# Kernel optimization log

Hardware: AMD Instinct MI355X
Metric: run time of the kernel (lower is better)

The kernel has to match this reference:

```python
import jax, jax.numpy as jnp
import numpy as np

HID, HEADS, NL, WIN = 512, 4, 2, 5
DH = HID // HEADS
SLOPE = 0.2
EPS = 1e-5
B, L = 16, 1024
NEG_INF = -1e30


def _layer_norm(x, g, b):
    m = jnp.mean(x, axis=-1, keepdims=True)
    v = jnp.mean(jnp.square(x - m), axis=-1, keepdims=True)
    return (x - m) * jax.lax.rsqrt(v + EPS) * g + b


def _build_masks(attention_mask, last_starts, seq_len):
    # node layout: [g, h_1..h_T, l], total N = seq_len + 2
    bsz = attention_mask.shape[0]
    N = seq_len + 2
    pos = jnp.arange(N)
    last = last_starts[:, None, None]  # (B,1,1)
    global_mask = jnp.ones((bsz, 1, N), jnp.float32)
    # local node: g, itself, and tokens of the last utterance (node idx last+1 .. seq_len)
    local_mask = ((pos == 0) | (pos == N - 1) | ((pos >= last + 1) & (pos <= seq_len))).astype(jnp.float32)  # (B,1,N)
    # token nodes: global node + window of neighboring tokens
    ii = jnp.arange(seq_len)[:, None]          # query token index
    jj = jnp.arange(N)[None, :]                # key node index
    t = jj - 1                                 # token index of key node (valid in [0, seq_len))
    win = (t >= 0) & (t < seq_len) & (jnp.abs(ii - t) <= WIN)
    base = (jj == 0) | win                     # (L,N)
    # tokens at/after last utterance start also attend to the local node
    to_local = (jnp.arange(seq_len)[None, :, None] >= last_starts[:, None, None]) & (jj[None] == N - 1)  # (B,L,N)
    token_mask = (base[None] | to_local).astype(jnp.float32)
    # padding: key tokens masked by attention_mask; g and l always visible; padded queries fully masked
    ones_col = jnp.ones((bsz, seq_len, 1), jnp.float32)
    pad = jnp.concatenate([ones_col, jnp.broadcast_to(attention_mask[:, None, :], (bsz, seq_len, seq_len)), ones_col], axis=-1)
    token_mask = token_mask * pad * attention_mask[:, :, None]
    return global_mask, local_mask, token_mask


def _gat(q, kv, W, a, mask):
    # W: (hid, hid) as torch Linear weight (out,in); a: (H, 2*DH)
    bsz, Lq, _ = q.shape
    N = kv.shape[1]
    Q = (q @ W.T).reshape(bsz, Lq, HEADS, DH)
    K = (kv @ W.T).reshape(bsz, N, HEADS, DH)
    V = K  # key==value tensor in this module, same projection
    # additive score decomposes: (a . [Q||K]) = Q.a_q + K.a_k
    sq = jnp.einsum('bqhd,hd->bhq', Q, a[:, :DH])
    sk = jnp.einsum('bkhd,hd->bhk', K, a[:, DH:])
    s = sq[:, :, :, None] + sk[:, :, None, :]           # (B,H,Lq,N)
    s = jnp.where(s >= 0, s, SLOPE * s)                 # LeakyReLU
    s = jnp.where(mask[:, None, :, :] > 0, s, NEG_INF)
    w = jax.nn.softmax(s, axis=-1)
    w = jnp.where(jnp.isnan(w), 0.0, w)
    out = jnp.einsum('bhqk,bkhd->bqhd', w, V)
    return out.reshape(bsz, Lq, HID)


def setup_inputs() -> dict:
    key = jax.random.key(0)
    ks = jax.random.split(key, 10)
    scale = 1.0 / np.sqrt(HID)
    return {
        'global_embedding': jax.random.normal(ks[0], (B, HID), jnp.float32),
        'token_embeddings': jax.random.normal(ks[1], (B, L, HID), jnp.float32),
        'local_embedding': jax.random.normal(ks[2], (B, HID), jnp.float32),
        'attention_mask': jnp.ones((B, L), jnp.float32),
        'last_utterance_starts': jax.random.randint(ks[3], (B,), 0, 512, jnp.int32),
        'gat_W': jax.random.normal(ks[4], (NL, HID, HID), jnp.float32) * scale,
        'gat_a': jax.random.normal(ks[5], (NL, HEADS, 2 * DH), jnp.float32) * scale,
        'ln_gamma': jnp.ones((NL, HID), jnp.float32),
        'ln_beta': jnp.zeros((NL, HID), jnp.float32),
        'ffn_w1': jax.random.normal(ks[6], (3, HID, 4 * HID), jnp.float32) * scale,
        'ffn_b1': jnp.zeros((3, 4 * HID), jnp.float32),
        'ffn_w2': jax.random.normal(ks[7], (3, 4 * HID, HID), jnp.float32) * (1.0 / np.sqrt(4 * HID)),
        'ffn_b2': jnp.zeros((3, HID), jnp.float32),
        'out_ln_gamma': jnp.ones((3, HID), jnp.float32),
        'out_ln_beta': jnp.zeros((3, HID), jnp.float32),
    }


def reference(global_embedding, token_embeddings, local_embedding, attention_mask,
              last_utterance_starts, gat_W, gat_a, ln_gamma, ln_beta,
              ffn_w1, ffn_b1, ffn_w2, ffn_b2, out_ln_gamma, out_ln_beta):
    bsz, seq_len, _ = token_embeddings.shape
    gm, lm, tm = _build_masks(attention_mask, last_utterance_starts, seq_len)
    g = global_embedding[:, None, :]
    h = token_embeddings
    l = local_embedding[:, None, :]
    nodes = jnp.concatenate([g, h, l], axis=1)
    for k in range(NL):
        g_new = jax.nn.elu(_gat(g, nodes, gat_W[k], gat_a[k], gm))
        h_new = jax.nn.elu(_gat(h, nodes, gat_W[k], gat_a[k], tm))
        l_new = jax.nn.elu(_gat(l, nodes, gat_W[k], gat_a[k], lm))
        g = _layer_norm(g + g_new, ln_gamma[k], ln_beta[k])
        h = _layer_norm(h + h_new, ln_gamma[k], ln_beta[k])
        l = _layer_norm(l + l_new, ln_gamma[k], ln_beta[k])
        nodes = jnp.concatenate([g, h, l], axis=1)
    def ffn(x, i):
        hmid = jax.nn.gelu(x @ ffn_w1[i] + ffn_b1[i], approximate=False)
        return hmid @ ffn_w2[i] + ffn_b2[i]
    g = g + ffn(g, 0)
    h = h + ffn(h, 1)
    l = l + ffn(l, 2)
    updated_global = _layer_norm(g[:, 0], out_ln_gamma[0], out_ln_beta[0])
    updated_tokens = _layer_norm(h, out_ln_gamma[1], out_ln_beta[1])
    updated_local = _layer_norm(l[:, 0], out_ln_gamma[2], out_ln_beta[2])
    return updated_global, updated_tokens, updated_local
```

## Files before the change

### kernel.cpp

```cpp
#include <hip/hip_runtime.h>
#include <stdint.h>
#include <math.h>

#define HIDN 512
#define NHEAD 4
#define DHEAD 128
#define BATCH 16
#define SEQ 1024
#define NNODE 1026
#define MROWS (BATCH * NNODE)
#define MPAD 16512
#define MTOK (BATCH * SEQ)
#define FFD 2048
#define JCH 114

typedef short bf16x8 __attribute__((ext_vector_type(8)));
typedef float f32x4 __attribute__((ext_vector_type(4)));

__device__ __forceinline__ float bf2f(ushort u) {
    union { uint32_t i; float f; } v; v.i = ((uint32_t)u) << 16; return v.f;
}
__device__ __forceinline__ ushort f2bf(float f) {
    uint32_t x = __float_as_uint(f);
    return (ushort)((x + 0x7fffu + ((x >> 16) & 1u)) >> 16);
}
__device__ __forceinline__ float gelu(float v) {
    float z = v * 0.70710678118654752f;
    float az = fabsf(z);
    float t = __builtin_amdgcn_rcpf(1.f + 0.3275911f * az);
    float y = ((((1.061405429f * t - 1.453152027f) * t + 1.421413741f) * t
                - 0.284496736f) * t + 0.254829592f) * t;
    float e = __expf(-az * az);
    float erfv = 1.f - y * e;
    erfv = (z >= 0.f) ? erfv : -erfv;
    return 0.5f * v * (1.f + erfv);
}
__device__ __forceinline__ int cswz(int row, int col) {
    return row * 128 + ((((col >> 2) ^ (row & 7)) & 31) << 2) + (col & 3);
}

__global__ __launch_bounds__(256) void k_build_nodes(
    const float* __restrict__ g, const float* __restrict__ tok,
    const float* __restrict__ l, ushort* __restrict__ nb)
{
    int idx = blockIdx.x * 256 + threadIdx.x;
    int r = idx >> 9, c = idx & 511;
    float u = 0.f;
    if (r < MROWS) {
        int b = r / NNODE;
        int n = r - b * NNODE;
        if (n == 0)            u = g[b * HIDN + c];
        else if (n <= SEQ)     u = tok[((size_t)b * SEQ + (n - 1)) * HIDN + c];
        else                   u = l[b * HIDN + c];
    }
    nb[idx] = f2bf(u);
}

__global__ __launch_bounds__(256) void k_cvt(
    const float* __restrict__ in, ushort* __restrict__ out, int n)
{
    int idx = blockIdx.x * 256 + threadIdx.x;
    if (idx < n) out[idx] = f2bf(in[idx]);
}

__global__ __launch_bounds__(256) void k_transpose(
    const float* __restrict__ in, ushort* __restrict__ out, int R, int C)
{
    __shared__ float t[32][33];
    int x = blockIdx.x * 32 + threadIdx.x;
    int y0 = blockIdx.y * 32;
    for (int dy = threadIdx.y; dy < 32; dy += 8)
        t[dy][threadIdx.x] = in[(size_t)(y0 + dy) * C + x];
    __syncthreads();
    int ox = y0 + threadIdx.x;
    int oy0 = blockIdx.x * 32;
    for (int dy = threadIdx.y; dy < 32; dy += 8)
        out[(size_t)(oy0 + dy) * R + ox] = f2bf(t[threadIdx.x][dy]);
}

#define BM 128
#define BN 128
#define BK 64

__global__ __launch_bounds__(256) void k_gemm_bt(
    const ushort* __restrict__ A, const ushort* __restrict__ Bt,
    float* __restrict__ Cf, ushort* __restrict__ Cb,
    const float* __restrict__ bias,
    int N, int K, int ldb, int mode, int amap, int mguard, int first)
{
    __shared__ ushort smem[2 * (BM * BK + BN * BK)];
    int tid = threadIdx.x;
    int lane = tid & 63;
    int wave = tid >> 6;
    int wm = wave >> 1, wn = wave & 1;

    int GX = gridDim.x;
    int nwg = GX * gridDim.y;
    int bid = blockIdx.y * GX + blockIdx.x;
    int q = nwg >> 3, r = nwg & 7;
    int xcd = bid & 7, pos = bid >> 3;
    int cbase = (xcd < r) ? xcd * (q + 1) : r * (q + 1) + (xcd - r) * q;
    int wk = cbase + pos;
    int m0 = (wk / GX) * BM;
    int n0 = (wk % GX) * BN;

    f32x4 acc[4][4];
#pragma unroll
    for (int i = 0; i < 4; ++i)
#pragma unroll
        for (int j = 0; j < 4; ++j) acc[i][j] = (f32x4){0.f, 0.f, 0.f, 0.f};

    int lr = lane >> 3;
    int gco = ((lane & 7) ^ lr) * 8;

    const ushort* pA[4];
    const ushort* pB[4];
#pragma unroll
    for (int u = 0; u < 4; ++u) {
        int qq = wave * 4 + u;
        int rr8 = qq * 8 + lr;
        int grA = m0 + rr8;
        if (amap) grA = grA + 2 * (grA >> 10) + 1;
        pA[u] = A + (size_t)grA * K + gco;
        int grB = n0 + rr8;
        pB[u] = Bt + (size_t)grB * ldb + gco;
    }

    auto stage = [&](int buf) {
        ushort* sA = smem + buf * (BM * BK + BN * BK);
        ushort* sB = sA + BM * BK;
#pragma unroll
        for (int u = 0; u < 4; ++u) {
            int qq = wave * 4 + u;
            __builtin_amdgcn_global_load_lds(
                (const __attribute__((address_space(1))) void*)pA[u],
                (__attribute__((address_space(3))) void*)&sA[qq * 512], 16, 0, 0);
            __builtin_amdgcn_global_load_lds(
                (const __attribute__((address_space(1))) void*)pB[u],
                (__attribute__((address_space(3))) void*)&sB[qq * 512], 16, 0, 0);
            pA[u] += BK;
            pB[u] += BK;
        }
    };

    const int nk = K / BK;
    stage(0);
    __syncthreads();

    int rr = lane & 7;
    int rhi = (lane & 15) >> 3;
    for (int t = 0; t < nk; ++t) {
        if (t + 1 < nk) stage((t + 1) & 1);

        const ushort* sAr = smem + (t & 1) * (BM * BK + BN * BK);
        const ushort* sBr = sAr + BM * BK;
#pragma unroll
        for (int kk = 0; kk < BK; kk += 32) {
            int c4 = (kk >> 3) + (lane >> 4);
            int swz = rr * 64 + ((c4 ^ rr) << 3);
            bf16x8 af[4], bfr[4];
#pragma unroll
            for (int i = 0; i < 4; ++i)
                af[i] = *reinterpret_cast<const bf16x8*>(&sAr[(wm * 8 + i * 2 + rhi) * 512 + swz]);
#pragma unroll
            for (int j = 0; j < 4; ++j)
                bfr[j] = *reinterpret_cast<const bf16x8*>(&sBr[(wn * 8 + j * 2 + rhi) * 512 + swz]);
#pragma unroll
            for (int i = 0; i < 4; ++i)
#pragma unroll
                for (int j = 0; j < 4; ++j)
                    acc[i][j] = __builtin_amdgcn_mfma_f32_16x16x32_bf16(af[i], bfr[j], acc[i][j], 0, 0, 0);
        }
        asm volatile("s_waitcnt vmcnt(0)" ::: "memory");
        __builtin_amdgcn_s_barrier();
    }
    __syncthreads();

    float* sC = (float*)smem;
    int rb = (lane >> 4) * 4;
    int cb = lane & 15;
    int lrow = tid >> 2;
    int lcol = (tid & 3) << 5;
#pragma unroll
    for (int pass = 0; pass < 2; ++pass) {
        if (wm == pass) {
#pragma unroll
            for (int i = 0; i < 4; ++i)
#pragma unroll
                for (int j = 0; j < 4; ++j)
#pragma unroll
                    for (int rg = 0; rg < 4; ++rg)
                        sC[cswz(i * 16 + rb + rg, wn * 64 + j * 16 + cb)] = acc[i][j][rg];
        }
        __syncthreads();
        int gm = m0 + pass * 64 + lrow;
        if (gm < mguard) {
            int gn0 = n0 + lcol;
            float v[32];
#pragma unroll
            for (int e4 = 0; e4 < 8; ++e4) {
                float4 t = *(const float4*)&sC[cswz(lrow, lcol + e4 * 4)];
                v[e4 * 4 + 0] = t.x; v[e4 * 4 + 1] = t.y;
                v[e4 * 4 + 2] = t.z; v[e4 * 4 + 3] = t.w;
            }
            if (mode == 1 || mode == 3) {
                if (mode == 3) {
                    const float* a1 = bias + (gn0 >> 7) * 256 + (gn0 & 127);
                    const float* a2 = a1 + 128;
                    float s1 = 0.f, s2 = 0.f;
#pragma unroll
                    for (int j = 0; j < 32; ++j) {
                        s1 += v[j] * a1[j];
                        s2 += v[j] * a2[j];
                    }
                    s1 += __shfl_xor(s1, 1); s1 += __shfl_xor(s1, 2);
                    s2 += __shfl_xor(s2, 1); s2 += __shfl_xor(s2, 2);
                    if ((tid & 3) == 0) {
                        Cf[gm * 4 + (gn0 >> 7)] = s1;
                        Cf[(size_t)MPAD * 4 + gm * 4 + (gn0 >> 7)] = s2;
                    }
                }
                uint4* dst = (uint4*)(Cb + (size_t)gm * N + gn0);
#pragma unroll
                for (int q2 = 0; q2 < 4; ++q2) {
                    float s[8];
#pragma unroll
                    for (int t = 0; t < 8; ++t) {
                        float x = v[q2 * 8 + t];
                        s[t] = (mode == 1) ? gelu(x + bias[gn0 + q2 * 8 + t]) : x;
                    }
                    uint4 w;
                    w.x = (uint32_t)f2bf(s[0]) | ((uint32_t)f2bf(s[1]) << 16);
                    w.y = (uint32_t)f2bf(s[2]) | ((uint32_t)f2bf(s[3]) << 16);
                    w.z = (uint32_t)f2bf(s[4]) | ((uint32_t)f2bf(s[5]) << 16);
                    w.w = (uint32_t)f2bf(s[6]) | ((uint32_t)f2bf(s[7]) << 16);
                    dst[q2] = w;
                }
            } else {
                float4* dst = (float4*)(Cf + (size_t)gm * N + gn0);
#pragma unroll
                for (int e4 = 0; e4 < 8; ++e4) {
                    float4 t;
                    t.x = v[e4 * 4 + 0]; t.y = v[e4 * 4 + 1];
                    t.z = v[e4 * 4 + 2]; t.w = v[e4 * 4 + 3];
                    if (!first) {
                        float4 o = dst[e4];
                        t.x += o.x; t.y += o.y; t.z += o.z; t.w += o.w;
                    }
                    dst[e4] = t;
                }
            }
        }
        __syncthreads();
    }
}

__global__ __launch_bounds__(256) void k_attn_token(
    const ushort* __restrict__ P, const float* __restrict__ sq, const float* __restrict__ sk,
    const float* __restrict__ am, const int* __restrict__ last,
    const float* __restrict__ gam, const float* __restrict__ bet,
    ushort* __restrict__ nb)
{
    int wid = blockIdx.x * 4 + (threadIdx.x >> 6);
    int tokid = ((wid & 7) << 11) | (wid >> 3);
    int b = tokid >> 10, i = tokid & 1023;
    int lane = threadIdx.x & 63;
    int hh = lane >> 4;
    int base = b * NNODE;
    int qrow = base + 1 + i;

    int kr[13];
    int val[13];
    int rowok = am[b * SEQ + i] > 0.f ? 1 : 0;
    kr[0] = base; val[0] = rowok;
#pragma unroll
    for (int s = 0; s < 11; ++s) {
        int t = i - 5 + s;
        int inb = (t >= 0) && (t <= SEQ - 1);
        int tt = inb ? t : 0;
        int v = inb && rowok && (am[b * SEQ + tt] > 0.f);
        kr[1 + s] = base + 1 + tt;
        val[1 + s] = v;
    }
    kr[12] = base + SEQ + 1;
    val[12] = (rowok && (i >= last[b])) ? 1 : 0;

    float sqv = sq[qrow * 4 + hh];
    float sc[13];
    float mx = -1e30f;
#pragma unroll
    for (int t = 0; t < 13; ++t) {
        float s = 0.f;
        if (val[t]) {
            s = sqv + sk[kr[t] * 4 + hh];
            s = s >= 0.f ? s : 0.2f * s;
            mx = fmaxf(mx, s);
        }
        sc[t] = s;
    }
    float den = 0.f;
#pragma unroll
    for (int t = 0; t < 13; ++t) {
        float ev = 0.f;
        if (val[t]) ev = expf(sc[t] - mx);
        sc[t] = ev; den += ev;
    }
    float inv = (den > 1e-30f && den < 1e30f) ? 1.f / den : 0.f;

    int o0 = lane * 8;
    float accv[8] = {0.f, 0.f, 0.f, 0.f, 0.f, 0.f, 0.f, 0.f};
#pragma unroll
    for (int t = 0; t < 13; ++t) {
        if (val[t]) {
            float wgt = sc[t] * inv;
            const ushort* pv = P + (size_t)kr[t] * HIDN + o0;
#pragma unroll
            for (int d = 0; d < 8; ++d) accv[d] += wgt * bf2f(pv[d]);
        }
    }

    ushort* nrow = nb + (size_t)qrow * HIDN + o0;
    float x[8], s1 = 0.f, s2 = 0.f;
#pragma unroll
    for (int d = 0; d < 8; ++d) {
        float v = accv[d];
        v = v > 0.f ? v : expf(v) - 1.f;
        v += bf2f(nrow[d]);
        x[d] = v; s1 += v; s2 += v * v;
    }
#pragma unroll
    for (int off = 32; off; off >>= 1) { s1 += __shfl_xor(s1, off); s2 += __shfl_xor(s2, off); }
    float mean = s1 * (1.f / 512.f);
    float var = s2 * (1.f / 512.f) - mean * mean; var = fmaxf(var, 0.f);
    float rn = rsqrtf(var + 1e-5f);
#pragma unroll
    for (int d = 0; d < 8; ++d) {
        float y = (x[d] - mean) * rn * gam[o0 + d] + bet[o0 + d];
        nrow[d] = f2bf(y);
    }
}

__global__ __launch_bounds__(256) void k_glsm(
    const float* __restrict__ sq, const float* __restrict__ sk,
    const int* __restrict__ last,
    float* __restrict__ ebuf, float* __restrict__ einv)
{
    __shared__ float red[1024];
    int rw = blockIdx.x, b = rw >> 1, isl = rw & 1;
    int base = b * NNODE;
    int qrow = base + (isl ? (SEQ + 1) : 0);
    int lastb = last[b];
    int tid = threadIdx.x;

    float sqh[4];
#pragma unroll
    for (int h = 0; h < 4; ++h) sqh[h] = sq[qrow * 4 + h];

    float mx[4] = {-1e30f, -1e30f, -1e30f, -1e30f};
    for (int j = tid; j < NNODE; j += 256) {
        bool ok = !isl || (j == 0 || j == SEQ + 1 || (j >= lastb + 1 && j <= SEQ));
        if (ok) {
#pragma unroll
            for (int h = 0; h < 4; ++h) {
                float s = sqh[h] + sk[(base + j) * 4 + h];
                s = s >= 0.f ? s : 0.2f * s;
                mx[h] = fmaxf(mx[h], s);
            }
        }
    }
#pragma unroll
    for (int h = 0; h < 4; ++h) red[tid * 4 + h] = mx[h];
    __syncthreads();
    for (int s = 128; s; s >>= 1) {
        if (tid < s) {
#pragma unroll
            for (int h = 0; h < 4; ++h)
                red[tid * 4 + h] = fmaxf(red[tid * 4 + h], red[(tid + s) * 4 + h]);
        }
        __syncthreads();
    }
#pragma unroll
    for (int h = 0; h < 4; ++h) mx[h] = red[h];
    __syncthreads();

    float sm[4] = {0.f, 0.f, 0.f, 0.f};
    for (int j = tid; j < NNODE; j += 256) {
        bool ok = !isl || (j == 0 || j == SEQ + 1 || (j >= lastb + 1 && j <= SEQ));
#pragma unroll
        for (int h = 0; h < 4; ++h) {
            float v = 0.f;
            if (ok) {
                float s = sqh[h] + sk[(base + j) * 4 + h];
                s = s >= 0.f ? s : 0.2f * s;
                v = expf(s - mx[h]);
            }
            ebuf[((size_t)rw * NNODE + j) * 4 + h] = v;
            sm[h] += v;
        }
    }
#pragma unroll
    for (int h = 0; h < 4; ++h) red[tid * 4 + h] = sm[h];
    __syncthreads();
    for (int s = 128; s; s >>= 1) {
        if (tid < s) {
#pragma unroll
            for (int h = 0; h < 4; ++h) red[tid * 4 + h] += red[(tid + s) * 4 + h];
        }
        __syncthreads();
    }
    if (tid < 4) {
        float den = red[tid];
        einv[rw * 4 + tid] = (den > 1e-30f && den < 1e30f) ? 1.f / den : 0.f;
    }
}

__global__ __launch_bounds__(256) void k_glpv(
    const ushort* __restrict__ P, const float* __restrict__ ebuf,
    float* __restrict__ pout2)
{
    __shared__ float es[JCH * 4];
    int p = blockIdx.x, rw = blockIdx.y;
    int b = rw >> 1;
    int base = b * NNODE;
    int tid = threadIdx.x;
    for (int t = tid; t < JCH * 4; t += 256)
        es[t] = ebuf[((size_t)rw * NNODE + p * JCH) * 4 + t];
    __syncthreads();
    int o0 = tid, o1 = tid + 256;
    int h0 = o0 >> 7, h1 = o1 >> 7;
    const ushort* Pb = P + (size_t)(base + p * JCH) * HIDN;
    float a0 = 0.f, a1 = 0.f;
    for (int j = 0; j < JCH; ++j) {
        const ushort* pr = Pb + (size_t)j * HIDN;
        a0 += es[j * 4 + h0] * bf2f(pr[o0]);
        a1 += es[j * 4 + h1] * bf2f(pr[o1]);
    }
    float* o = pout2 + ((size_t)rw * 9 + p) * HIDN;
    o[o0] = a0;
    o[o1] = a1;
}

__global__ __launch_bounds__(256) void k_glred(
    const float* __restrict__ pout2, const float* __restrict__ einv,
    const float* __restrict__ gam, const float* __restrict__ bet,
    ushort* __restrict__ nb)
{
    __shared__ float red[512];
    int rw = blockIdx.x, b = rw >> 1, isl = rw & 1;
    size_t qrow = (size_t)b * NNODE + (isl ? SEQ + 1 : 0);
    int tid = threadIdx.x;
    float xv[2], s1 = 0.f, s2 = 0.f;
#pragma unroll
    for (int u = 0; u < 2; ++u) {
        int o = tid + u * 256;
        int h = o >> 7;
        float acc = 0.f;
#pragma unroll
        for (int p = 0; p < 9; ++p)
            acc += pout2[((size_t)rw * 9 + p) * HIDN + o];
        acc *= einv[rw * 4 + h];
        float v = acc > 0.f ? acc : expf(acc) - 1.f;
        v += bf2f(nb[qrow * HIDN + o]);
        xv[u] = v; s1 += v; s2 += v * v;
    }
    red[tid] = s1;
    __syncthreads();
    for (int s = 128; s; s >>= 1) { if (tid < s) red[tid] += red[tid + s]; __syncthreads(); }
    float mean = red[0] * (1.f / 512.f);
    __syncthreads();
    red[tid] = s2;
    __syncthreads();
    for (int s = 128; s; s >>= 1) { if (tid < s) red[tid] += red[tid + s]; __syncthreads(); }
    float var = red[0] * (1.f / 512.f) - mean * mean; var = fmaxf(var, 0.f);
    float rn = rsqrtf(var + 1e-5f);
#pragma unroll
    for (int u = 0; u < 2; ++u) {
        int o = tid + u * 256;
        float y = (xv[u] - mean) * rn * gam[o] + bet[o];
        nb[qrow * HIDN + o] = f2bf(y);
    }
}

__global__ __launch_bounds__(256) void k_fgl1(
    const ushort* __restrict__ nb, const float* __restrict__ w1,
    float* __restrict__ pmid)
{
    __shared__ float xs[64];
    int p = blockIdx.x, rw = blockIdx.y;
    int b = rw >> 1, isl = rw & 1;
    int idx = isl ? 2 : 0;
    size_t nrow = (size_t)b * NNODE + (isl ? SEQ + 1 : 0);
    int tid = threadIdx.x;
    if (tid < 64) xs[tid] = bf2f(nb[nrow * HIDN + p * 64 + tid]);
    __syncthreads();
    const float* W1 = w1 + (size_t)idx * HIDN * FFD + (size_t)p * 64 * FFD;
    float acc[8] = {0.f, 0.f, 0.f, 0.f, 0.f, 0.f, 0.f, 0.f};
    for (int ii = 0; ii < 64; ++ii) {
        float xv = xs[ii];
        const float* wrow = W1 + (size_t)ii * FFD + tid;
#pragma unroll
        for (int u = 0; u < 8; ++u) acc[u] += xv * wrow[u * 256];
    }
    float* o = pmid + ((size_t)rw * 8 + p) * FFD + tid;
#pragma unroll
    for (int u = 0; u < 8; ++u) o[u * 256] = acc[u];
}

__global__ __launch_bounds__(256) void k_fgl2(
    const float* __restrict__ pmid, const float* __restrict__ b1,
    float* __restrict__ mid)
{
    int g = blockIdx.x * 256 + threadIdx.x;
    int e4 = g * 4;
    int rw = e4 >> 11;
    int m = e4 & 2047;
    int isl = rw & 1;
    int idx = isl ? 2 : 0;
#pragma unroll
    for (int d = 0; d < 4; ++d) {
        float s = 0.f;
#pragma unroll
        for (int p = 0; p < 8; ++p)
            s += pmid[((size_t)rw * 8 + p) * FFD + m + d];
        s += b1[idx * FFD + m + d];
        mid[(size_t)rw * FFD + m + d] = gelu(s);
    }
}

__global__ __launch_bounds__(256) void k_fgl3(
    const float* __restrict__ mid, const float* __restrict__ w2,
    float* __restrict__ pout)
{
    __shared__ float ms[256];
    int p = blockIdx.x, rw = blockIdx.y;
    int isl = rw & 1;
    int idx = isl ? 2 : 0;
    int tid = threadIdx.x;
    ms[tid] = mid[(size_t)rw * FFD + p * 256 + tid];
    __syncthreads();
    const float* W2 = w2 + (size_t)idx * FFD * HIDN + (size_t)p * 256 * HIDN;
    float a0 = 0.f, a1 = 0.f;
    for (int mm = 0; mm < 256; ++mm) {
        float mv = ms[mm];
        const float* wrow = W2 + (size_t)mm * HIDN + tid;
        a0 += mv * wrow[0];
        a1 += mv * wrow[256];
    }
    float* o = pout + ((size_t)rw * 8 + p) * HIDN + tid;
    o[0] = a0;
    o[256] = a1;
}

__global__ __launch_bounds__(256) void k_fgl4(
    const float* __restrict__ pout, const float* __restrict__ b2,
    const ushort* __restrict__ nb,
    const float* __restrict__ og, const float* __restrict__ obt,
    float* __restrict__ out)
{
    __shared__ float red[512];
    int rw = blockIdx.x;
    int b = rw >> 1, isl = rw & 1;
    int idx = isl ? 2 : 0;
    size_t nrow = (size_t)b * NNODE + (isl ? SEQ + 1 : 0);
    int tid = threadIdx.x;
    float xv[2], s1 = 0.f, s2 = 0.f;
#pragma unroll
    for (int u = 0; u < 2; ++u) {
        int o = tid + u * 256;
        float s = 0.f;
#pragma unroll
        for (int p = 0; p < 8; ++p)
            s += pout[((size_t)rw * 8 + p) * HIDN + o];
        s += b2[idx * HIDN + o] + bf2f(nb[nrow * HIDN + o]);
        xv[u] = s; s1 += s; s2 += s * s;
    }
    red[tid] = s1;
    __syncthreads();
    for (int s = 128; s; s >>= 1) { if (tid < s) red[tid] += red[tid + s]; __syncthreads(); }
    float mean = red[0] * (1.f / 512.f);
    __syncthreads();
    red[tid] = s2;
    __syncthreads();
    for (int s = 128; s; s >>= 1) { if (tid < s) red[tid] += red[tid + s]; __syncthreads(); }
    float var = red[0] * (1.f / 512.f) - mean * mean; var = fmaxf(var, 0.f);
    float rn = rsqrtf(var + 1e-5f);
    size_t obase = isl ? ((size_t)8192 + (size_t)MTOK * HIDN + (size_t)b * HIDN)
                       : ((size_t)b * HIDN);
#pragma unroll
    for (int u = 0; u < 2; ++u) {
        int o = tid + u * 256;
        out[obase + o] = (xv[u] - mean) * rn * og[idx * HIDN + o] + obt[idx * HIDN + o];
    }
}

__global__ __launch_bounds__(64) void k_ln_final(
    float* __restrict__ Pt, const ushort* __restrict__ nb,
    const float* __restrict__ b2,
    const float* __restrict__ gam, const float* __restrict__ bet)
{
    int r = blockIdx.x, lane = threadIdx.x;
    int nrow = r + 2 * (r >> 10) + 1;
    int o0 = lane * 8;
    float* x = Pt + (size_t)r * HIDN + o0;
    const ushort* res = nb + (size_t)nrow * HIDN + o0;
    float v[8], s1 = 0.f, s2 = 0.f;
#pragma unroll
    for (int d = 0; d < 8; ++d) {
        float t = x[d] + b2[o0 + d] + bf2f(res[d]);
        v[d] = t; s1 += t; s2 += t * t;
    }
#pragma unroll
    for (int off = 32; off; off >>= 1) { s1 += __shfl_xor(s1, off); s2 += __shfl_xor(s2, off); }
    float mean = s1 * (1.f / 512.f);
    float var = s2 * (1.f / 512.f) - mean * mean; var = fmaxf(var, 0.f);
    float rn = rsqrtf(var + 1e-5f);
#pragma unroll
    for (int d = 0; d < 8; ++d)
        x[d] = (v[d] - mean) * rn * gam[o0 + d] + bet[o0 + d];
}

extern "C" void kernel_launch(void* const* d_in, const int* in_sizes, int n_in,
                              void* d_out, int out_size, void* d_ws, size_t ws_size,
                              hipStream_t stream)
{
    (void)in_sizes; (void)n_in; (void)out_size; (void)ws_size;
    const float* g_emb   = (const float*)d_in[0];
    const float* tok_emb = (const float*)d_in[1];
    const float* l_emb   = (const float*)d_in[2];
    const float* am      = (const float*)d_in[3];
    const int*   last    = (const int*)d_in[4];
    const float* gat_W   = (const float*)d_in[5];
    const float* gat_a   = (const float*)d_in[6];
    const float* ln_g    = (const float*)d_in[7];
    const float* ln_b    = (const float*)d_in[8];
    const float* ffn_w1  = (const float*)d_in[9];
    const float* ffn_b1  = (const float*)d_in[10];
    const float* ffn_w2  = (const float*)d_in[11];
    const float* ffn_b2  = (const float*)d_in[12];
    const float* oln_g   = (const float*)d_in[13];
    const float* oln_b   = (const float*)d_in[14];
    float* out = (float*)d_out;

    char* w = (char*)d_ws;
    ushort* nodes_b = (ushort*)w; w += (size_t)MPAD * HIDN * 2;
    char*   scratch = w;          w += (size_t)8 * 1024 * 1024;
    ushort* w1t     = (ushort*)w; w += (size_t)FFD * HIDN * 2;
    ushort* w2t     = (ushort*)w; w += (size_t)FFD * HIDN * 2;
    ushort* gatWb   = (ushort*)w; w += (size_t)2 * HIDN * HIDN * 2;
    float*  sqb     = (float*)w;  w += (size_t)MPAD * 4 * 4;
    float*  skb     = (float*)w;  w += (size_t)MPAD * 4 * 4;
    ushort* Hmid    = (ushort*)w; w += (size_t)MTOK * FFD * 2;

    float* pmid = (float*)scratch;
    float* mid  = pmid + (size_t)32 * 8 * FFD;
    float* pout = mid + (size_t)32 * FFD;
    float* ebuf  = (float*)(scratch + (size_t)3 * 1024 * 1024);
    float* einv  = ebuf + (size_t)32 * NNODE * 4;
    float* pout2 = einv + 128;

    ushort* P = (ushort*)out;
    float* Pt = out + 8192;

    k_build_nodes<<<MPAD * HIDN / 256, 256, 0, stream>>>(g_emb, tok_emb, l_emb, nodes_b);
    k_cvt<<<(2 * HIDN * HIDN) / 256, 256, 0, stream>>>(gat_W, gatWb, 2 * HIDN * HIDN);
    k_transpose<<<dim3(FFD / 32, HIDN / 32), dim3(32, 8), 0, stream>>>(ffn_w1 + (size_t)HIDN * FFD, w1t, HIDN, FFD);
    k_transpose<<<dim3(HIDN / 32, FFD / 32), dim3(32, 8), 0, stream>>>(ffn_w2 + (size_t)FFD * HIDN, w2t, FFD, HIDN);

    for (int k = 0; k < 2; ++k) {
        k_gemm_bt<<<dim3(HIDN / BN, MPAD / BM), 256, 0, stream>>>(
            nodes_b, gatWb + (size_t)k * HIDN * HIDN, sqb, P,
            gat_a + k * NHEAD * 2 * DHEAD,
            HIDN, HIDN, HIDN, 3, 0, MROWS, 1);
        k_attn_token<<<MTOK / 4, 256, 0, stream>>>(P, sqb, skb, am, last,
                                                   ln_g + k * HIDN, ln_b + k * HIDN, nodes_b);
        k_glsm<<<32, 256, 0, stream>>>(sqb, skb, last, ebuf, einv);
        k_glpv<<<dim3(9, 32), 256, 0, stream>>>(P, ebuf, pout2);
        k_glred<<<32, 256, 0, stream>>>(pout2, einv, ln_g + k * HIDN, ln_b + k * HIDN, nodes_b);
    }

    k_fgl1<<<dim3(8, 32), 256, 0, stream>>>(nodes_b, ffn_w1, pmid);
    k_fgl2<<<64, 256, 0, stream>>>(pmid, ffn_b1, mid);
    k_fgl3<<<dim3(8, 32), 256, 0, stream>>>(mid, ffn_w2, pout);
    k_fgl4<<<32, 256, 0, stream>>>(pout, ffn_b2, nodes_b, oln_g, oln_b, out);

    k_gemm_bt<<<dim3(FFD / BN, MTOK / BM), 256, 0, stream>>>(
        nodes_b, w1t, nullptr, Hmid,
        ffn_b1 + FFD, FFD, HIDN, HIDN, 1, 1, MTOK, 1);
    k_gemm_bt<<<dim3(HIDN / BN, MTOK / BM), 256, 0, stream>>>(
        Hmid, w2t, Pt, nullptr, nullptr,
        HIDN, FFD, FFD, 0, 0, MTOK, 1);
    k_ln_final<<<MTOK, 64, 0, stream>>>(Pt, nodes_b, ffn_b2 + HIDN, oln_g + HIDN, oln_b + HIDN);
}
```

Before: 496.1 us.

## Add 256x256-tile GEMM with direct global-to-LDS loads for token FFN

Introduces a new 512-thread GEMM kernel with 256x256 output tiles, double-buffered LDS staging via global_load_lds, XOR-swizzled shared layout, and a block-index remap for L2 locality. The two token-FFN GEMMs switch to it, fusing bias+GELU in the first. Larger tiles raise arithmetic intensity and cut global traffic, at the cost of 128 KB LDS per block and fewer blocks (the second GEMM launches only 128), which limits occupancy.

```diff
diff --git a/kernel.cpp b/kernel.cpp
--- a/kernel.cpp
+++ b/kernel.cpp
@@ -249,6 +249,162 @@
                     }
                     dst[e4] = t;
                 }
+            }
+        }
+        __syncthreads();
+    }
+}
+
+#define QK 64
+
+__global__ __launch_bounds__(512) void k_gemm256(
+    const ushort* __restrict__ A, const ushort* __restrict__ Bt,
+    float* __restrict__ Cf, ushort* __restrict__ Cb,
+    const float* __restrict__ bias,
+    int N, int K, int mode, int amap)
+{
+    extern __shared__ ushort smem[];
+    int tid = threadIdx.x;
+    int lane = tid & 63;
+    int wave = tid >> 6;
+    int wr = wave >> 2;
+    int wc = wave & 3;
+
+    int GX = gridDim.x;
+    int nwg = GX * gridDim.y;
+    int bid = blockIdx.y * GX + blockIdx.x;
+    int cpx = nwg >> 3;
+    int wk = (bid & 7) * cpx + (bid >> 3);
+    int m0 = (wk / GX) * 256;
+    int n0 = (wk % GX) * 256;
+
+    f32x4 acc[8][4];
+#pragma unroll
+    for (int i = 0; i < 8; ++i)
+#pragma unroll
+        for (int j = 0; j < 4; ++j) acc[i][j] = (f32x4){0.f, 0.f, 0.f, 0.f};
+
+    int lr = lane >> 3;
+    int gco = ((lane & 7) ^ lr) * 8;
+
+    const ushort* pA[4];
+    const ushort* pB[4];
+#pragma unroll
+    for (int u = 0; u < 4; ++u) {
+        int q = wave * 4 + u;
+        int grA = m0 + q * 8 + lr;
+        if (amap) grA = grA + 2 * (grA >> 10) + 1;
+        pA[u] = A + (size_t)grA * K + gco;
+        int grB = n0 + q * 8 + lr;
+        pB[u] = Bt + (size_t)grB * K + gco;
+    }
+
+    auto stage = [&](int buf) {
+        ushort* sA = smem + buf * 32768;
+        ushort* sB = sA + 16384;
+#pragma unroll
+        for (int u = 0; u < 4; ++u) {
+            int q = wave * 4 + u;
+            __builtin_amdgcn_global_load_lds(
+                (const __attribute__((address_space(1))) void*)pA[u],
+                (__attribute__((address_space(3))) void*)&sA[q * 512], 16, 0, 0);
+            __builtin_amdgcn_global_load_lds(
+                (const __attribute__((address_space(1))) void*)pB[u],
+                (__attribute__((address_space(3))) void*)&sB[q * 512], 16, 0, 0);
+            pA[u] += QK;
+            pB[u] += QK;
+        }
+    };
+
+    const int nk = K / QK;
+    stage(0);
+    __syncthreads();
+
+    int rr = lane & 7;
+    int rhi = (lane & 15) >> 3;
+    for (int t = 0; t < nk; ++t) {
+        if (t + 1 < nk) stage((t + 1) & 1);
+
+        const ushort* sAr = smem + (t & 1) * 32768;
+        const ushort* sBr = sAr + 16384;
+#pragma unroll
+        for (int qd = 0; qd < 4; ++qd) {
+            int fi0 = (qd & 1) * 4;
+            int fj0 = (qd >> 1) * 2;
+#pragma unroll
+            for (int kk = 0; kk < 2; ++kk) {
+                int c4 = kk * 4 + (lane >> 4);
+                int swz = rr * 64 + ((c4 ^ rr) << 3);
+                bf16x8 af[4], bfr[2];
+#pragma unroll
+                for (int i = 0; i < 4; ++i) {
+                    int qA = wr * 16 + (fi0 + i) * 2 + rhi;
+                    af[i] = *reinterpret_cast<const bf16x8*>(&sAr[qA * 512 + swz]);
+                }
+#pragma unroll
+                for (int j = 0; j < 2; ++j) {
+                    int qB = wc * 8 + (fj0 + j) * 2 + rhi;
+                    bfr[j] = *reinterpret_cast<const bf16x8*>(&sBr[qB * 512 + swz]);
+                }
+#pragma unroll
+                for (int i = 0; i < 4; ++i)
+#pragma unroll
+                    for (int j = 0; j < 2; ++j)
+                        acc[fi0 + i][fj0 + j] = __builtin_amdgcn_mfma_f32_16x16x32_bf16(
+                            af[i], bfr[j], acc[fi0 + i][fj0 + j], 0, 0, 0);
+            }
+        }
+        __syncthreads();
+    }
+
+    float* sC = (float*)smem;
+    int rb = (lane >> 4) * 4;
+    int cb = lane & 15;
+    int lrow = tid >> 2;
+    int lcol = (tid & 3) << 6;
+#pragma unroll
+    for (int pass = 0; pass < 2; ++pass) {
+        if (wr == pass) {
+#pragma unroll
+            for (int fi = 0; fi < 8; ++fi)
+#pragma unroll
+                for (int fj = 0; fj < 4; ++fj)
+#pragma unroll
+                    for (int rg = 0; rg < 4; ++rg) {
+                        int row = fi * 16 + rb + rg;
+                        int col = wc * 64 + fj * 16 + cb;
+                        sC[row * 256 + ((((col >> 2) ^ (row & 7)) & 63) << 2) + (col & 3)] =
+                            acc[fi][fj][rg];
+                    }
+        }
+        __syncthreads();
+        int gm = m0 + pass * 128 + lrow;
+        if (mode == 1) {
+            uint4* dst = (uint4*)(Cb + (size_t)gm * N + n0 + lcol);
+#pragma unroll
+            for (int g = 0; g < 8; ++g) {
+                int col = lcol + g * 8;
+                float4 a = *(const float4*)&sC[lrow * 256 + ((((col >> 2) ^ (lrow & 7)) & 63) << 2)];
+                float4 b = *(const float4*)&sC[lrow * 256 + (((((col + 4) >> 2) ^ (lrow & 7)) & 63) << 2)];
+                const float* bp = bias + n0 + col;
+                float s0 = gelu(a.x + bp[0]), s1 = gelu(a.y + bp[1]);
+                float s2 = gelu(a.z + bp[2]), s3 = gelu(a.w + bp[3]);
+                float s4 = gelu(b.x + bp[4]), s5 = gelu(b.y + bp[5]);
+                float s6 = gelu(b.z + bp[6]), s7 = gelu(b.w + bp[7]);
+                uint4 w;
+                w.x = (uint32_t)f2bf(s0) | ((uint32_t)f2bf(s1) << 16);
+                w.y = (uint32_t)f2bf(s2) | ((uint32_t)f2bf(s3) << 16);
+                w.z = (uint32_t)f2bf(s4) | ((uint32_t)f2bf(s5) << 16);
+                w.w = (uint32_t)f2bf(s6) | ((uint32_t)f2bf(s7) << 16);
+                dst[g] = w;
+            }
+        } else {
+            float4* dst = (float4*)(Cf + (size_t)gm * N + n0 + lcol);
+#pragma unroll
+            for (int e4 = 0; e4 < 16; ++e4) {
+                int col = lcol + e4 * 4;
+                float4 tv = *(const float4*)&sC[lrow * 256 + ((((col >> 2) ^ (lrow & 7)) & 63) << 2)];
+                dst[e4] = tv;
             }
         }
         __syncthreads();
@@ -683,11 +839,9 @@
     k_fgl3<<<dim3(8, 32), 256, 0, stream>>>(mid, ffn_w2, pout);
     k_fgl4<<<32, 256, 0, stream>>>(pout, ffn_b2, nodes_b, oln_g, oln_b, out);
 
-    k_gemm_bt<<<dim3(FFD / BN, MTOK / BM), 256, 0, stream>>>(
-        nodes_b, w1t, nullptr, Hmid,
-        ffn_b1 + FFD, FFD, HIDN, HIDN, 1, 1, MTOK, 1);
-    k_gemm_bt<<<dim3(HIDN / BN, MTOK / BM), 256, 0, stream>>>(
-        Hmid, w2t, Pt, nullptr, nullptr,
-        HIDN, FFD, FFD, 0, 0, MTOK, 1);
+    k_gemm256<<<dim3(FFD / 256, MTOK / 256), 512, 131072, stream>>>(
+        nodes_b, w1t, nullptr, Hmid, ffn_b1 + FFD, FFD, HIDN, 1, 1);
+    k_gemm256<<<dim3(HIDN / 256, MTOK / 256), 512, 131072, stream>>>(
+        Hmid, w2t, Pt, nullptr, nullptr, HIDN, FFD, 0, 0);
     k_ln_final<<<MTOK, 64, 0, stream>>>(Pt, nodes_b, ffn_b2 + HIDN, oln_g + HIDN, oln_b + HIDN);
 }
```

New measurement: 486.8 us. About the same (-1.9%).
